# Performance work log

Measured on AMD Instinct MI355X. Metric: run time of the kernel, lower is better.

## Reference

```python
import jax, jax.numpy as jnp
import numpy as np
from jax.scipy.special import logsumexp

EPSILON = 0.01        # temperature
DIST_THRESH = 0.2
NUM_ITERS = 3
NEG_INF = -1.0e9

B, N, M, C = 4, 4096, 4096, 256


def setup_inputs() -> dict:
    key = jax.random.key(0)
    k1, k2, k3, k4, k5 = jax.random.split(key, 5)
    source_feats = jax.random.normal(k1, (B, N, C), dtype=jnp.float32)
    source_locs = jax.random.uniform(k2, (B, N, 2), dtype=jnp.float32)
    target_locs = jax.random.uniform(k3, (B, M, 2), dtype=jnp.float32)
    source_valid_mask = jax.random.bernoulli(k4, 0.9, (B, N))
    target_valid_mask = jax.random.bernoulli(k5, 0.9, (B, M))
    return {
        "source_feats": source_feats,
        "source_locs": source_locs,
        "target_locs": target_locs,
        "source_valid_mask": source_valid_mask,
        "target_valid_mask": target_valid_mask,
    }


def reference(source_feats, source_locs, target_locs, source_valid_mask, target_valid_mask):
    # pairwise squared distances: [B, M, N]
    diff = target_locs[:, :, None, :] - source_locs[:, None, :, :]  # [B, M, N, 2]
    dist_sq = jnp.sum(diff * diff, axis=-1)                          # [B, M, N]
    log_K = -dist_sq / (EPSILON + 1e-8)

    valid_connection = dist_sq < (DIST_THRESH ** 2)
    valid_connection = valid_connection & source_valid_mask[:, None, :]
    valid_connection = valid_connection & target_valid_mask[:, :, None]
    log_K = jnp.where(valid_connection, log_K, NEG_INF)

    # Sinkhorn iterations in log space
    v = jnp.zeros((log_K.shape[0], 1, log_K.shape[2]), dtype=log_K.dtype)  # [B,1,N]
    u = jnp.zeros((log_K.shape[0], log_K.shape[1], 1), dtype=log_K.dtype)  # [B,M,1]
    for _ in range(NUM_ITERS):
        u = -logsumexp(log_K + v, axis=2, keepdims=True)
        v = -logsumexp(log_K + u, axis=1, keepdims=True)
        v = jnp.where(source_valid_mask[:, None, :], v, 0.0)

    attn = jnp.exp(log_K + u + v)  # [B, M, N]
    attn = jax.lax.stop_gradient(attn)  # original computes it under torch.no_grad

    target_feats = jnp.einsum('bmn,bnc->bmc', attn, source_feats)
    target_feats = target_feats * target_valid_mask[:, :, None].astype(target_feats.dtype)
    has_source = jnp.any(valid_connection, axis=-1, keepdims=True)
    target_feats = target_feats * has_source.astype(target_feats.dtype)
    return target_feats
```

## Files before the change

### kernel.cpp

```cpp
#include <hip/hip_runtime.h>
#include <math.h>

#define BB 4
#define BN 4096
#define CC 256
constexpr float T2      = 0.04f;
constexpr float INV_EPS = (float)(1.0 / 0.01000001);

__device__ __forceinline__ int cell_of(float x, float y) {
  int cx = (int)(x * 5.0f); cx = cx < 0 ? 0 : (cx > 4 ? 4 : cx);
  int cy = (int)(y * 5.0f); cy = cy < 0 ? 0 : (cy > 4 ? 4 : cy);
  return cy * 5 + cx;
}

__device__ __forceinline__ void dma16(const void* g, void* l) {
  __builtin_amdgcn_global_load_lds(
      (const __attribute__((address_space(1))) void*)g,
      (__attribute__((address_space(3))) void*)l, 16, 0, 0);
}

__global__ __launch_bounds__(256) void k_bin(
    const float* __restrict__ tlocs, const float* __restrict__ slocs,
    const int* __restrict__ tmask, const int* __restrict__ smask,
    int* __restrict__ Zc,
    int* __restrict__ starts_t, int* __restrict__ starts_s,
    int* __restrict__ perm_t, int* __restrict__ perm_s,
    float4* __restrict__ t_sorted, float4* __restrict__ s_sorted) {
  const int which = blockIdx.x & 1, b = blockIdx.x >> 1;
  const float* locs = which ? slocs : tlocs;
  const int*   mask = which ? smask : tmask;
  int* starts       = which ? starts_s : starts_t;
  int* perm         = which ? perm_s : perm_t;
  float4* pack      = which ? s_sorted : t_sorted;
  const int tid = threadIdx.x;
  if (blockIdx.x == 0) Zc[tid] = 0;
  __shared__ int cnt[25];
  __shared__ int st[26];
  __shared__ int cur[25];
  if (tid < 25) cnt[tid] = 0;
  __syncthreads();
  for (int i = tid; i < BN; i += 256)
    atomicAdd(&cnt[cell_of(locs[(b * BN + i) * 2], locs[(b * BN + i) * 2 + 1])], 1);
  __syncthreads();
  if (tid == 0) {
    int acc = 0;
    for (int c = 0; c < 25; c++) { st[c] = acc; acc += cnt[c]; }
    st[25] = acc;
  }
  __syncthreads();
  if (tid < 25) cur[tid] = st[tid];
  if (tid < 26) starts[b * 32 + tid] = st[tid];
  __syncthreads();
  for (int i = tid; i < BN; i += 256) {
    float x = locs[(b * BN + i) * 2], y = locs[(b * BN + i) * 2 + 1];
    int pos = atomicAdd(&cur[cell_of(x, y)], 1);
    perm[b * BN + pos] = i;
    pack[b * BN + pos] = make_float4(x, y, 0.f, mask[b * BN + i] ? 1.f : 0.f);
  }
}

__global__ __launch_bounds__(256) void k_sink(const float4* __restrict__ opp,
                                              float4* __restrict__ own,
                                              const int* __restrict__ opp_starts,
                                              const int* __restrict__ Zin,
                                              int* __restrict__ Zout,
                                              int zero_invalid) {
  const int wv   = threadIdx.x >> 6;
  const int lane = threadIdx.x & 63;
  const int rowb = blockIdx.x * 16 + wv * 4;
  const int b    = rowb >> 12;
  float4 me[4];
  float  s[4] = {0.f, 0.f, 0.f, 0.f};
  int ryLo = 5, ryHi = -1, rxLo = 5, rxHi = -1;
  #pragma unroll
  for (int i = 0; i < 4; i++) {
    me[i] = own[rowb + i];
    if (me[i].w != 0.f) {
      int cell = cell_of(me[i].x, me[i].y);
      int cy = cell / 5, cx = cell % 5;
      ryLo = min(ryLo, max(cy - 1, 0)); ryHi = max(ryHi, min(cy + 1, 4));
      rxLo = min(rxLo, max(cx - 1, 0)); rxHi = max(rxHi, min(cx + 1, 4));
    }
  }
  for (int ry = ryLo; ry <= ryHi; ry++) {
    const int r0 = opp_starts[b * 32 + ry * 5 + rxLo];
    const int r1 = opp_starts[b * 32 + ry * 5 + rxHi + 1];
    for (int j = r0 + lane; j < r1; j += 64) {
      float4 o = opp[b * BN + j];
      #pragma unroll
      for (int i = 0; i < 4; i++) {
        float dx = me[i].x - o.x, dy = me[i].y - o.y;
        float d2 = fmaf(dx, dx, dy * dy);
        bool  c  = (d2 < T2) && (o.w != 0.f) && (me[i].w != 0.f);
        float t  = c ? fmaf(d2, -INV_EPS, o.z) : -3e30f;
        s[i] += __expf(t);
      }
    }
  }
  #pragma unroll
  for (int i = 0; i < 4; i++)
    for (int off = 32; off > 0; off >>= 1) s[i] += __shfl_xor(s[i], off);
  if (lane == 0) {
    const float Zf = (float)Zin[b];
    #pragma unroll
    for (int i = 0; i < 4; i++) {
      float ss  = s[i] + Zf;
      float val = (ss > 0.f) ? -logf(ss) : 1.0e9f;
      if (zero_invalid && me[i].w == 0.f) val = 0.f;
      own[rowb + i] = make_float4(me[i].x, me[i].y, val, me[i].w);
      if (val == 1.0e9f) atomicAdd(&Zout[b], 1);
    }
  }
}

#define MAXCH 12
#define CH 16

__global__ __launch_bounds__(256) void k_out(
    const float* __restrict__ feats, const float4* __restrict__ t_sorted,
    const float4* __restrict__ s_sorted, const int* __restrict__ perm_t,
    const int* __restrict__ perm_s, const int* __restrict__ starts_t,
    const int* __restrict__ starts_s, float* __restrict__ out) {
  const int b = blockIdx.z;
  const int cell = blockIdx.y / 3, rsel = blockIdx.y % 3;
  const int cy = cell / 5, cx = cell % 5;
  const int ry = cy + rsel - 1;
  if (ry < 0 || ry > 4) return;
  const int t0 = starts_t[b * 32 + cell], t1 = starts_t[b * 32 + cell + 1];
  const int base = t0 + blockIdx.x * 32;
  if (base >= t1) return;
  const int rx0 = max(cx - 1, 0), rx1 = min(cx + 1, 4);
  const int s0 = starts_s[b * 32 + ry * 5 + rx0];
  const int s1 = starts_s[b * 32 + ry * 5 + rx1 + 1];
  if (s0 >= s1) return;
  const int nt = min(32, t1 - base);

  __shared__ float4 tL[32];
  __shared__ int    morg[32];
  __shared__ __align__(16) float attnL[16 * 36];
  __shared__ __align__(16) float fL[2 * CH * 256];

  const int tid  = threadIdx.x;
  const int lane = tid & 63;
  const int w    = tid >> 6;

  if (tid < 32) {
    if (tid < nt) {
      tL[tid]   = t_sorted[b * BN + base + tid];
      morg[tid] = perm_t[b * BN + base + tid];
    } else {
      tL[tid]   = make_float4(0.f, 0.f, 0.f, 0.f);
      morg[tid] = 0;
    }
  }
  __syncthreads();

  const int tmg  = tid >> 5;
  const int chg  = tid & 31;
  const int tmp_ = w * 8 + (lane & 7);
  const int nnA  = lane >> 3, nnB = nnA + 8;
  const float4 t4p = tL[tmp_];
  const int sB = b * BN;

  float4 psA = s_sorted[sB + min(s0 + nnA, s1 - 1)];
  float4 psB = s_sorted[sB + min(s0 + nnB, s1 - 1)];
  float4 pnA, pnB;
  int sidxN[4];
  {
    int s0i[4];
    #pragma unroll
    for (int q = 0; q < 4; q++)
      s0i[q] = perm_s[sB + min(s0 + q * 4 + w, s1 - 1)];
    #pragma unroll
    for (int q = 0; q < 4; q++)
      dma16((const char*)feats + ((size_t)((b << 12) + s0i[q]) << 10) + (size_t)lane * 16,
            (void*)&fL[(q * 4 + w) * 256]);
    #pragma unroll
    for (int q = 0; q < 4; q++)
      sidxN[q] = perm_s[sB + min(s0 + CH + q * 4 + w, s1 - 1)];
  }

  float acc[4][8];
  #pragma unroll
  for (int i = 0; i < 4; i++)
    #pragma unroll
    for (int j = 0; j < 8; j++) acc[i][j] = 0.f;

  int bb = 0;
  for (int n0 = s0; n0 < s1; n0 += CH, bb ^= 1) {
    asm volatile("s_waitcnt vmcnt(0)" ::: "memory");
    __builtin_amdgcn_s_barrier();
    __builtin_amdgcn_sched_barrier(0);
    const int n1 = n0 + CH;
    const bool more = (n1 < s1);
    if (more) {
      #pragma unroll
      for (int q = 0; q < 4; q++)
        dma16((const char*)feats + ((size_t)((b << 12) + sidxN[q]) << 10) + (size_t)lane * 16,
              (void*)&fL[((bb ^ 1) * CH + q * 4 + w) * 256]);
      pnA = s_sorted[sB + min(n1 + nnA, s1 - 1)];
      pnB = s_sorted[sB + min(n1 + nnB, s1 - 1)];
      #pragma unroll
      for (int q = 0; q < 4; q++)
        sidxN[q] = perm_s[sB + min(n1 + CH + q * 4 + w, s1 - 1)];
    }
    {
      float dx = t4p.x - psA.x, dy = t4p.y - psA.y;
      float d2 = fmaf(dx, dx, dy * dy);
      bool  c  = (n0 + nnA < s1) && (d2 < T2) && (psA.w != 0.f) && (t4p.w != 0.f);
      attnL[nnA * 36 + tmp_] = c ? __expf(fmaf(d2, -INV_EPS, t4p.z + psA.z)) : 0.f;
      dx = t4p.x - psB.x; dy = t4p.y - psB.y;
      d2 = fmaf(dx, dx, dy * dy);
      c  = (n0 + nnB < s1) && (d2 < T2) && (psB.w != 0.f) && (t4p.w != 0.f);
      attnL[nnB * 36 + tmp_] = c ? __expf(fmaf(d2, -INV_EPS, t4p.z + psB.z)) : 0.f;
    }
    const float* fb = &fL[bb * CH * 256];
    #pragma unroll 4
    for (int nn = 0; nn < 16; nn++) {
      const float4 av = *(const float4*)&attnL[nn * 36 + tmg * 4];
      const float4 f0 = *(const float4*)&fb[nn * 256 + chg * 4];
      const float4 f1 = *(const float4*)&fb[nn * 256 + 128 + chg * 4];
      float avv[4] = {av.x, av.y, av.z, av.w};
      float ff[8]  = {f0.x, f0.y, f0.z, f0.w, f1.x, f1.y, f1.z, f1.w};
      #pragma unroll
      for (int i = 0; i < 4; i++)
        #pragma unroll
        for (int j = 0; j < 8; j++)
          acc[i][j] = fmaf(avv[i], ff[j], acc[i][j]);
    }
    if (more) { psA = pnA; psB = pnB; }
  }
  #pragma unroll
  for (int i = 0; i < 4; i++) {
    int tm = tmg * 4 + i;
    if (tm < nt) {
      float* op = out + (((b << 12) + morg[tm]) << 8) + chg * 4;
      #pragma unroll
      for (int j = 0; j < 4; j++) atomicAdd(op + j,       acc[i][j]);
      #pragma unroll
      for (int j = 0; j < 4; j++) atomicAdd(op + 128 + j, acc[i][j + 4]);
    }
  }
}

extern "C" void kernel_launch(void* const* d_in, const int* in_sizes, int n_in,
                              void* d_out, int out_size, void* d_ws, size_t ws_size,
                              hipStream_t stream) {
  const float* feats = (const float*)d_in[0];
  const float* slocs = (const float*)d_in[1];
  const float* tlocs = (const float*)d_in[2];
  const int*   smask = (const int*)d_in[3];
  const int*   tmask = (const int*)d_in[4];
  float* out = (float*)d_out;

  char* ws = (char*)d_ws;
  int*    Zc       = (int*)(ws + 1024);
  int*    starts_t = (int*)(ws + 2048);
  int*    starts_s = (int*)(ws + 2560);
  int*    perm_t   = (int*)(ws + 4096);
  int*    perm_s   = (int*)(ws + 69632);
  float4* s_sorted = (float4*)(ws + 135168);
  float4* t_sorted = (float4*)(ws + 397312);

  hipMemsetAsync(out, 0, (size_t)out_size * sizeof(float), stream);
  k_bin<<<8, 256, 0, stream>>>(tlocs, slocs, tmask, smask, Zc,
                               starts_t, starts_s, perm_t, perm_s,
                               t_sorted, s_sorted);
  for (int it = 0; it < 3; it++) {
    k_sink<<<1024, 256, 0, stream>>>(s_sorted, t_sorted, starts_s,
                                     Zc + (it == 0 ? 0 : (2 * it) * 4),
                                     Zc + (2 * it + 1) * 4, 0);
    k_sink<<<1024, 256, 0, stream>>>(t_sorted, s_sorted, starts_t,
                                     Zc + (2 * it + 1) * 4,
                                     Zc + (2 * it + 2) * 4, 1);
  }
  k_out<<<dim3(MAXCH, 75, BB), 256, 0, stream>>>(feats, t_sorted, s_sorted,
                                                 perm_t, perm_s, starts_t,
                                                 starts_s, out);
}
```

Baseline: 572.4 us.

## Use split-bf16 MFMA for output GEMM with pre-permuted packed feature tiles

Adds a pack kernel that gathers source features into sorted order and splits each float into high and low bf16 halves, stored in a swizzled 16-row tile layout. The output kernel then builds attention tiles in registers and runs the product on 32x32x16 bf16 MFMA using three products (hi*hi, hi*lo, lo*hi) to approximate fp32 accuracy, replacing the scalar FMA loop. Results are staged through LDS before the atomic adds. This removes the per-row gather indirection and the CUDA-core FMA cost, at the price of an extra pack pass over the features, more MFMA work, and slightly lower precision.

```diff
diff --git a/kernel.cpp b/kernel.cpp
--- a/kernel.cpp
+++ b/kernel.cpp
@@ -6,6 +6,9 @@
 #define CC 256
 constexpr float T2      = 0.04f;
 constexpr float INV_EPS = (float)(1.0 / 0.01000001);
+
+typedef __attribute__((ext_vector_type(8)))  short bf16x8;
+typedef __attribute__((ext_vector_type(16))) float f32x16;
 
 __device__ __forceinline__ int cell_of(float x, float y) {
   int cx = (int)(x * 5.0f); cx = cx < 0 ? 0 : (cx > 4 ? 4 : cx);
@@ -59,6 +62,41 @@
   }
 }
 
+__global__ __launch_bounds__(256) void k_pack(
+    const float* __restrict__ feats, const int* __restrict__ perm_s,
+    unsigned* __restrict__ fB) {
+  const int b   = blockIdx.x >> 8;
+  const int blk = blockIdx.x & 255;
+  const int tid = threadIdx.x;
+  __shared__ float fs[16][260];
+  __shared__ int   sidx[16];
+  if (tid < 16) sidx[tid] = perm_s[b * BN + blk * 16 + tid];
+  __syncthreads();
+  #pragma unroll
+  for (int q = 0; q < 4; q++) {
+    int idx = q * 256 + tid;
+    int r = idx >> 6, c4 = idx & 63;
+    float4 v = ((const float4*)feats)[(((b << 12) + sidx[r]) << 6) + c4];
+    fs[r][c4 * 4 + 0] = v.x; fs[r][c4 * 4 + 1] = v.y;
+    fs[r][c4 * 4 + 2] = v.z; fs[r][c4 * 4 + 3] = v.w;
+  }
+  __syncthreads();
+  const int ch = tid;
+  unsigned* dst = fB + ((((size_t)b << 8) + blk) << 12) + ch * 16;
+  unsigned pk[16];
+  #pragma unroll
+  for (int sl = 0; sl < 16; sl++) {
+    float f = fs[sl][ch];
+    unsigned fb = __float_as_uint(f);
+    unsigned hb = fb & 0xFFFF0000u;
+    float lo = f - __uint_as_float(hb);
+    pk[sl ^ (((ch >> 1) & 3) << 2)] = hb | (__float_as_uint(lo) >> 16);
+  }
+  #pragma unroll
+  for (int q = 0; q < 4; q++)
+    ((uint4*)dst)[q] = make_uint4(pk[q*4], pk[q*4+1], pk[q*4+2], pk[q*4+3]);
+}
+
 __global__ __launch_bounds__(256) void k_sink(const float4* __restrict__ opp,
                                               float4* __restrict__ own,
                                               const int* __restrict__ opp_starts,
@@ -114,13 +152,12 @@
 }
 
 #define MAXCH 12
-#define CH 16
 
 __global__ __launch_bounds__(256) void k_out(
-    const float* __restrict__ feats, const float4* __restrict__ t_sorted,
+    const unsigned* __restrict__ fB, const float4* __restrict__ t_sorted,
     const float4* __restrict__ s_sorted, const int* __restrict__ perm_t,
-    const int* __restrict__ perm_s, const int* __restrict__ starts_t,
-    const int* __restrict__ starts_s, float* __restrict__ out) {
+    const int* __restrict__ starts_t, const int* __restrict__ starts_s,
+    float* __restrict__ out) {
   const int b = blockIdx.z;
   const int cell = blockIdx.y / 3, rsel = blockIdx.y % 3;
   const int cy = cell / 5, cx = cell % 5;
@@ -135,10 +172,9 @@
   if (s0 >= s1) return;
   const int nt = min(32, t1 - base);
 
+  __shared__ __align__(16) unsigned pool[8576];
   __shared__ float4 tL[32];
   __shared__ int    morg[32];
-  __shared__ __align__(16) float attnL[16 * 36];
-  __shared__ __align__(16) float fL[2 * CH * 256];
 
   const int tid  = threadIdx.x;
   const int lane = tid & 63;
@@ -155,90 +191,131 @@
   }
   __syncthreads();
 
-  const int tmg  = tid >> 5;
-  const int chg  = tid & 31;
-  const int tmp_ = w * 8 + (lane & 7);
-  const int nnA  = lane >> 3, nnB = nnA + 8;
-  const float4 t4p = tL[tmp_];
+  const int kg = lane >> 5;
+  const int ln = lane & 31;
+  const float4 t4a = tL[ln];
   const int sB = b * BN;
 
-  float4 psA = s_sorted[sB + min(s0 + nnA, s1 - 1)];
-  float4 psB = s_sorted[sB + min(s0 + nnB, s1 - 1)];
-  float4 pnA, pnB;
-  int sidxN[4];
+  const int blk0 = s0 >> 4;
+  const int nBlk = ((s1 + 15) >> 4) - blk0;
+
   {
-    int s0i[4];
+    const unsigned* g = fB + ((((size_t)b << 8) + blk0) << 12);
     #pragma unroll
     for (int q = 0; q < 4; q++)
-      s0i[q] = perm_s[sB + min(s0 + q * 4 + w, s1 - 1)];
-    #pragma unroll
-    for (int q = 0; q < 4; q++)
-      dma16((const char*)feats + ((size_t)((b << 12) + s0i[q]) << 10) + (size_t)lane * 16,
-            (void*)&fL[(q * 4 + w) * 256]);
-    #pragma unroll
-    for (int q = 0; q < 4; q++)
-      sidxN[q] = perm_s[sB + min(s0 + CH + q * 4 + w, s1 - 1)];
-  }
-
-  float acc[4][8];
-  #pragma unroll
-  for (int i = 0; i < 4; i++)
-    #pragma unroll
-    for (int j = 0; j < 8; j++) acc[i][j] = 0.f;
-
-  int bb = 0;
-  for (int n0 = s0; n0 < s1; n0 += CH, bb ^= 1) {
+      dma16(g + (w * 4 + q) * 256 + lane * 4,
+            (void*)(pool + (w * 4 + q) * 256));
+  }
+  float4 ps[8], pn[8];
+  {
+    int j0 = blk0 * 16 + kg * 8;
+    #pragma unroll
+    for (int e = 0; e < 8; e++)
+      ps[e] = s_sorted[sB + min(j0 + e, BN - 1)];
+  }
+
+  f32x16 acc0, acc1;
+  #pragma unroll
+  for (int i = 0; i < 16; i++) { acc0[i] = 0.f; acc1[i] = 0.f; }
+
+  int buf = 0;
+  for (int r = 0; r < nBlk; r++, buf ^= 1) {
     asm volatile("s_waitcnt vmcnt(0)" ::: "memory");
     __builtin_amdgcn_s_barrier();
     __builtin_amdgcn_sched_barrier(0);
-    const int n1 = n0 + CH;
-    const bool more = (n1 < s1);
+    const bool more = (r + 1 < nBlk);
     if (more) {
+      const unsigned* g = fB + ((((size_t)b << 8) + blk0 + r + 1) << 12);
       #pragma unroll
       for (int q = 0; q < 4; q++)
-        dma16((const char*)feats + ((size_t)((b << 12) + sidxN[q]) << 10) + (size_t)lane * 16,
-              (void*)&fL[((bb ^ 1) * CH + q * 4 + w) * 256]);
-      pnA = s_sorted[sB + min(n1 + nnA, s1 - 1)];
-      pnB = s_sorted[sB + min(n1 + nnB, s1 - 1)];
+        dma16(g + (w * 4 + q) * 256 + lane * 4,
+              (void*)(pool + (buf ^ 1) * 4096 + (w * 4 + q) * 256));
+      int j0n = (blk0 + r + 1) * 16 + kg * 8;
       #pragma unroll
-      for (int q = 0; q < 4; q++)
-        sidxN[q] = perm_s[sB + min(n1 + CH + q * 4 + w, s1 - 1)];
-    }
-    {
-      float dx = t4p.x - psA.x, dy = t4p.y - psA.y;
+      for (int e = 0; e < 8; e++)
+        pn[e] = s_sorted[sB + min(j0n + e, BN - 1)];
+    }
+    const int j0 = (blk0 + r) * 16 + kg * 8;
+    unsigned ahv[8], alv[8];
+    #pragma unroll
+    for (int e = 0; e < 8; e++) {
+      float4 s4 = ps[e];
+      int j = j0 + e;
+      float dx = t4a.x - s4.x, dy = t4a.y - s4.y;
       float d2 = fmaf(dx, dx, dy * dy);
-      bool  c  = (n0 + nnA < s1) && (d2 < T2) && (psA.w != 0.f) && (t4p.w != 0.f);
-      attnL[nnA * 36 + tmp_] = c ? __expf(fmaf(d2, -INV_EPS, t4p.z + psA.z)) : 0.f;
-      dx = t4p.x - psB.x; dy = t4p.y - psB.y;
-      d2 = fmaf(dx, dx, dy * dy);
-      c  = (n0 + nnB < s1) && (d2 < T2) && (psB.w != 0.f) && (t4p.w != 0.f);
-      attnL[nnB * 36 + tmp_] = c ? __expf(fmaf(d2, -INV_EPS, t4p.z + psB.z)) : 0.f;
-    }
-    const float* fb = &fL[bb * CH * 256];
-    #pragma unroll 4
-    for (int nn = 0; nn < 16; nn++) {
-      const float4 av = *(const float4*)&attnL[nn * 36 + tmg * 4];
-      const float4 f0 = *(const float4*)&fb[nn * 256 + chg * 4];
-      const float4 f1 = *(const float4*)&fb[nn * 256 + 128 + chg * 4];
-      float avv[4] = {av.x, av.y, av.z, av.w};
-      float ff[8]  = {f0.x, f0.y, f0.z, f0.w, f1.x, f1.y, f1.z, f1.w};
+      bool  c  = (j >= s0) && (j < s1) && (d2 < T2) &&
+                 (s4.w != 0.f) && (t4a.w != 0.f);
+      float a  = c ? __expf(fmaf(d2, -INV_EPS, t4a.z + s4.z)) : 0.f;
+      unsigned ab = __float_as_uint(a);
+      unsigned hb = ab & 0xFFFF0000u;
+      float alo = a - __uint_as_float(hb);
+      ahv[e] = ab >> 16;
+      alv[e] = __float_as_uint(alo) >> 16;
+    }
+    union { unsigned u[4]; bf16x8 v; } BH, BL;
+    #pragma unroll
+    for (int i = 0; i < 4; i++) {
+      BH.u[i] = ahv[2*i] | (ahv[2*i+1] << 16);
+      BL.u[i] = alv[2*i] | (alv[2*i+1] << 16);
+    }
+    const unsigned* tile = pool + buf * 4096;
+    #pragma unroll
+    for (int mt = 0; mt < 2; mt++) {
+      const int chl = w * 64 + mt * 32 + ln;
+      const int xv  = (chl >> 1) & 3;
+      const int g0  = ((kg << 1) | 0) ^ xv;
+      const int g1  = ((kg << 1) | 1) ^ xv;
+      union { uint4 q[2]; unsigned u[8]; } A;
+      A.q[0] = *(const uint4*)(tile + chl * 16 + g0 * 4);
+      A.q[1] = *(const uint4*)(tile + chl * 16 + g1 * 4);
+      union { unsigned u[4]; bf16x8 v; } AH, AL;
       #pragma unroll
-      for (int i = 0; i < 4; i++)
-        #pragma unroll
-        for (int j = 0; j < 8; j++)
-          acc[i][j] = fmaf(avv[i], ff[j], acc[i][j]);
-    }
-    if (more) { psA = pnA; psB = pnB; }
-  }
-  #pragma unroll
-  for (int i = 0; i < 4; i++) {
-    int tm = tmg * 4 + i;
-    if (tm < nt) {
-      float* op = out + (((b << 12) + morg[tm]) << 8) + chg * 4;
-      #pragma unroll
-      for (int j = 0; j < 4; j++) atomicAdd(op + j,       acc[i][j]);
-      #pragma unroll
-      for (int j = 0; j < 4; j++) atomicAdd(op + 128 + j, acc[i][j + 4]);
+      for (int i = 0; i < 4; i++) {
+        AH.u[i] = (A.u[2*i] >> 16)     | (A.u[2*i+1] & 0xFFFF0000u);
+        AL.u[i] = (A.u[2*i] & 0xFFFFu) | (A.u[2*i+1] << 16);
+      }
+      if (mt == 0) {
+        acc0 = __builtin_amdgcn_mfma_f32_32x32x16_bf16(AH.v, BH.v, acc0, 0, 0, 0);
+        acc0 = __builtin_amdgcn_mfma_f32_32x32x16_bf16(AH.v, BL.v, acc0, 0, 0, 0);
+        acc0 = __builtin_amdgcn_mfma_f32_32x32x16_bf16(AL.v, BH.v, acc0, 0, 0, 0);
+      } else {
+        acc1 = __builtin_amdgcn_mfma_f32_32x32x16_bf16(AH.v, BH.v, acc1, 0, 0, 0);
+        acc1 = __builtin_amdgcn_mfma_f32_32x32x16_bf16(AH.v, BL.v, acc1, 0, 0, 0);
+        acc1 = __builtin_amdgcn_mfma_f32_32x32x16_bf16(AL.v, BH.v, acc1, 0, 0, 0);
+      }
+    }
+    #pragma unroll
+    for (int e = 0; e < 8; e++) ps[e] = pn[e];
+  }
+
+  __syncthreads();
+  float* Dl = (float*)pool;
+  #pragma unroll
+  for (int mt = 0; mt < 2; mt++) {
+    #pragma unroll
+    for (int rg = 0; rg < 4; rg++) {
+      int chb = w * 64 + mt * 32 + 8 * rg + 4 * kg;
+      float4 v;
+      if (mt == 0) v = make_float4(acc0[rg*4], acc0[rg*4+1], acc0[rg*4+2], acc0[rg*4+3]);
+      else         v = make_float4(acc1[rg*4], acc1[rg*4+1], acc1[rg*4+2], acc1[rg*4+3]);
+      *(float4*)&Dl[ln * 268 + chb] = v;
+    }
+  }
+  __syncthreads();
+  {
+    const int tmg = tid >> 5, chg = tid & 31;
+    #pragma unroll
+    for (int i = 0; i < 4; i++) {
+      int tm = tmg * 4 + i;
+      if (tm < nt) {
+        float* op = out + (((b << 12) + morg[tm]) << 8) + chg * 4;
+        float4 d0 = *(float4*)&Dl[tm * 268 + chg * 4];
+        float4 d1 = *(float4*)&Dl[tm * 268 + 128 + chg * 4];
+        atomicAdd(op + 0, d0.x); atomicAdd(op + 1, d0.y);
+        atomicAdd(op + 2, d0.z); atomicAdd(op + 3, d0.w);
+        atomicAdd(op + 128, d1.x); atomicAdd(op + 129, d1.y);
+        atomicAdd(op + 130, d1.z); atomicAdd(op + 131, d1.w);
+      }
     }
   }
 }
@@ -261,11 +338,13 @@
   int*    perm_s   = (int*)(ws + 69632);
   float4* s_sorted = (float4*)(ws + 135168);
   float4* t_sorted = (float4*)(ws + 397312);
+  unsigned* fB     = (unsigned*)(ws + 663552);
 
   hipMemsetAsync(out, 0, (size_t)out_size * sizeof(float), stream);
   k_bin<<<8, 256, 0, stream>>>(tlocs, slocs, tmask, smask, Zc,
                                starts_t, starts_s, perm_t, perm_s,
                                t_sorted, s_sorted);
+  k_pack<<<1024, 256, 0, stream>>>(feats, perm_s, fB);
   for (int it = 0; it < 3; it++) {
     k_sink<<<1024, 256, 0, stream>>>(s_sorted, t_sorted, starts_s,
                                      Zc + (it == 0 ? 0 : (2 * it) * 4),
@@ -274,7 +353,7 @@
                                      Zc + (2 * it + 1) * 4,
                                      Zc + (2 * it + 2) * 4, 1);
   }
-  k_out<<<dim3(MAXCH, 75, BB), 256, 0, stream>>>(feats, t_sorted, s_sorted,
-                                                 perm_t, perm_s, starts_t,
-                                                 starts_s, out);
-}
+  k_out<<<dim3(MAXCH, 75, BB), 256, 0, stream>>>(fB, t_sorted, s_sorted,
+                                                 perm_t, starts_t, starts_s,
+                                                 out);
+}
```

Result: faster. 557.6 us (-2.6%).
